# Kernel tuning notes

Measured on AMD Instinct MI355X. Metric: run time of the kernel, lower is better.

The kernel has to match this reference:

```python
import jax, jax.numpy as jnp
import numpy as np

B, N, D, H = 4, 4096, 512, 512
EDGE_P = 0.01  # adjacency density


def _glorot(key, shape):
    fan_in, fan_out = shape
    limit = np.sqrt(6.0 / (fan_in + fan_out)).astype(np.float32)
    return jax.random.uniform(key, shape, jnp.float32, -limit, limit)


def setup_inputs() -> dict:
    key = jax.random.key(0)
    ks = jax.random.split(key, 9)
    batch_graph = jax.random.normal(ks[0], (B, N, D), jnp.float32)
    adj = (jax.random.uniform(ks[1], (B, N, N)) < EDGE_P).astype(jnp.float32)
    adj = jnp.minimum(adj + jnp.eye(N, dtype=jnp.float32)[None], 1.0)  # self loops, 0/1
    return {
        "batch_graph": batch_graph,
        "adj": adj,
        "W1": _glorot(ks[2], (D, H)), "b1": jnp.zeros((H,), jnp.float32),
        "W2": _glorot(ks[3], (H, H)), "b2": jnp.zeros((H,), jnp.float32),
        "W3": _glorot(ks[4], (H, D)), "b3": jnp.zeros((D,), jnp.float32),
    }


def _normalize_adj(adj):
    # Faithful to GCN.normalize_sparse_adj: D^{-1/2} A^T D^{-1/2}
    rowsum = adj.sum(axis=1)                       # [B, N] (sum over dim 1, as in torch)
    d_inv_sqrt = jnp.where(rowsum > 0, jax.lax.rsqrt(jnp.maximum(rowsum, 1e-30)), 0.0)
    # (A @ diag(d))^T @ diag(d)  ->  d_i * A[j,i] * d_j
    return d_inv_sqrt[:, :, None] * jnp.swapaxes(adj, 1, 2) * d_inv_sqrt[:, None, :]


def reference(batch_graph, adj, W1, b1, W2, b2, W3, b3):
    # Block-diagonal big_adj @ big_graph == independent per-batch matmuls;
    # we exploit that instead of materializing the [B*N, B*N] dense matrix.
    a = _normalize_adj(adj)                                   # [B, N, N]
    # GraphConvolution (pygcn-style): out = adj @ (x @ W) + b; dropout = identity (eval)
    h = jax.nn.relu(jnp.einsum('bij,bjd->bid', a, batch_graph @ W1) + b1)
    h = jax.nn.relu(jnp.einsum('bij,bjd->bid', a, h @ W2) + b2)
    out = jnp.einsum('bij,bjd->bid', a, h @ W3) + b3          # [B, N, D]
    return out
```

## Files before the change

kernel.cpp:

```cpp
#include <hip/hip_runtime.h>
#include <stdint.h>

#define CAP 128

typedef __attribute__((ext_vector_type(8))) short bf16x8;
typedef __attribute__((ext_vector_type(4))) float f32x4;

typedef __attribute__((address_space(3))) uint32_t lds_u32;
typedef __attribute__((address_space(1))) const uint32_t glb_u32;

__device__ __forceinline__ unsigned short f2bf(float f) {
  union { float f; uint32_t u; } c; c.f = f;
  return (unsigned short)((c.u + 0x7fffu + ((c.u >> 16) & 1u)) >> 16);
}
__device__ __forceinline__ float bf2f(uint32_t b) {
  union { uint32_t u; float f; } c; c.u = b << 16; return c.f;
}

__global__ __launch_bounds__(256) void k_detect(const uint32_t* __restrict__ a,
                                                int* __restrict__ flag) {
  int i = blockIdx.x * 256 + threadIdx.x;
  bool found = false;
  for (int k = 0; k < 64; k++) {
    uint32_t x = a[(size_t)k * 65536 + i];
    if (x == 0x00003F80u || x == 0x3F803F80u) found = true;
  }
  if (found) flag[0] = 1;
}

__global__ __launch_bounds__(256) void k_build(const void* __restrict__ adjp,
                                               int* __restrict__ cnt,
                                               int* __restrict__ cols,
                                               const int* __restrict__ flag) {
  int gid = blockIdx.x * 256 + threadIdx.x;
  if (flag[0]) {
    const uint4* a = (const uint4*)adjp;
    uint4 v = a[gid];
    int i0 = (gid & 511) * 8;
    int j  = (gid >> 9) & 4095;
    int b  = gid >> 21;
    int base = b << 12;
    uint32_t w[4] = {v.x, v.y, v.z, v.w};
#pragma unroll
    for (int q = 0; q < 4; q++) {
      if (w[q] & 0xffffu) {
        int c = base + i0 + q * 2;
        int p = atomicAdd(&cnt[c], 1);
        if (p < CAP) cols[(size_t)c * CAP + p] = j;
      }
      if (w[q] >> 16) {
        int c = base + i0 + q * 2 + 1;
        int p = atomicAdd(&cnt[c], 1);
        if (p < CAP) cols[(size_t)c * CAP + p] = j;
      }
    }
  } else {
    const float4* a = (const float4*)adjp;
#pragma unroll
    for (int it = 0; it < 2; it++) {
      int v4 = gid + it * 8388608;
      float4 v = a[v4];
      int i0 = (v4 & 1023) * 4;
      int j  = (v4 >> 10) & 4095;
      int b  = v4 >> 22;
      int base = b << 12;
      float e[4] = {v.x, v.y, v.z, v.w};
#pragma unroll
      for (int q = 0; q < 4; q++) {
        if (e[q] != 0.0f) {
          int c = base + i0 + q;
          int p = atomicAdd(&cnt[c], 1);
          if (p < CAP) cols[(size_t)c * CAP + p] = j;
        }
      }
    }
  }
}

__global__ __launch_bounds__(256) void k_dinv(const int* __restrict__ cnt,
                                              float* __restrict__ dinv) {
  int i = blockIdx.x * 256 + threadIdx.x;
  int c = cnt[i];
  dinv[i] = (c > 0) ? 1.0f / sqrtf((float)c) : 0.0f;
}

__global__ __launch_bounds__(256) void k_convx(const void* __restrict__ xp,
                                               ushort* __restrict__ xb,
                                               const int* __restrict__ flag) {
  int gid = blockIdx.x * 256 + threadIdx.x;
  if (flag[0]) {
    const uint4* in = (const uint4*)xp;
    ((uint4*)xb)[gid] = in[gid];
  } else {
    const float4* in = (const float4*)xp;
#pragma unroll
    for (int it = 0; it < 2; it++) {
      int i = gid + it * 1048576;
      float4 v = in[i];
      uint32_t lo = (uint32_t)f2bf(v.x) | ((uint32_t)f2bf(v.y) << 16);
      uint32_t hi = (uint32_t)f2bf(v.z) | ((uint32_t)f2bf(v.w) << 16);
      ((uint2*)xb)[i] = make_uint2(lo, hi);
    }
  }
}

__global__ __launch_bounds__(256) void k_wconv(const void* __restrict__ wp,
                                               ushort* __restrict__ wt,
                                               const int* __restrict__ flag) {
  int o = blockIdx.x * 256 + threadIdx.x;
  int n = o >> 9, k = o & 511;
  if (flag[0]) wt[o] = ((const ushort*)wp)[k * 512 + n];
  else         wt[o] = f2bf(((const float*)wp)[k * 512 + n]);
}

__global__ __launch_bounds__(256) void k_bconv(const void* __restrict__ bp,
                                               float* __restrict__ bf,
                                               const int* __restrict__ flag) {
  int i = blockIdx.x * 256 + threadIdx.x;
  bf[i] = flag[0] ? bf2f(((const ushort*)bp)[i]) : ((const float*)bp)[i];
}

__device__ __forceinline__ void gl_lds16(const ushort* g, ushort* l) {
  __builtin_amdgcn_global_load_lds((glb_u32*)g, (lds_u32*)l, 16, 0, 0);
}

__global__ __launch_bounds__(256) void k_gemm(const ushort* __restrict__ X,
                                              const ushort* __restrict__ WT,
                                              ushort* __restrict__ Z) {
  __shared__ ushort As[128 * 32];
  __shared__ ushort Bs[128 * 32];
  const int K = 512, NO = 512;
  int tid = threadIdx.x;
  int m0 = blockIdx.y * 128, n0 = blockIdx.x * 128;
  int lane = tid & 63;
  int wv = tid >> 6;
  int wm = (wv >> 1) << 6;
  int wn = (wv & 1) << 6;
  int lr = lane & 15;
  int lq = lane >> 4;

  f32x4 zero = {0.f, 0.f, 0.f, 0.f};
  f32x4 acc[4][4];
#pragma unroll
  for (int im = 0; im < 4; im++)
#pragma unroll
    for (int in_ = 0; in_ < 4; in_++) acc[im][in_] = zero;

  const ushort* Xg = X  + (size_t)(m0 + (tid >> 2)) * K + ((tid & 3) << 3);
  const ushort* Wg = WT + (size_t)(n0 + (tid >> 2)) * K + ((tid & 3) << 3);

  for (int kt = 0; kt < K; kt += 32) {
    __syncthreads();
    gl_lds16(Xg + kt,                    &As[tid * 8]);
    gl_lds16(Xg + kt + (size_t)64 * K,   &As[2048 + tid * 8]);
    gl_lds16(Wg + kt,                    &Bs[tid * 8]);
    gl_lds16(Wg + kt + (size_t)64 * K,   &Bs[2048 + tid * 8]);
    __syncthreads();
    bf16x8 af[4], bfr[4];
#pragma unroll
    for (int im = 0; im < 4; im++)
      af[im] = *(const bf16x8*)&As[(wm + im * 16 + lr) * 32 + lq * 8];
#pragma unroll
    for (int in_ = 0; in_ < 4; in_++)
      bfr[in_] = *(const bf16x8*)&Bs[(wn + in_ * 16 + lr) * 32 + lq * 8];
#pragma unroll
    for (int im = 0; im < 4; im++)
#pragma unroll
      for (int in_ = 0; in_ < 4; in_++)
        acc[im][in_] = __builtin_amdgcn_mfma_f32_16x16x32_bf16(
            af[im], bfr[in_], acc[im][in_], 0, 0, 0);
  }

#pragma unroll
  for (int im = 0; im < 4; im++) {
    int row0 = m0 + wm + im * 16 + lq * 4;
#pragma unroll
    for (int in_ = 0; in_ < 4; in_++) {
      int col = n0 + wn + in_ * 16 + lr;
#pragma unroll
      for (int r = 0; r < 4; r++)
        Z[(size_t)(row0 + r) * NO + col] = f2bf(acc[im][in_][r]);
    }
  }
}

__global__ __launch_bounds__(256) void k_spmm(const ushort* __restrict__ Z,
                                              const int* __restrict__ cnt,
                                              const int* __restrict__ cols,
                                              const float* __restrict__ dinv,
                                              const float* __restrict__ bias,
                                              void* __restrict__ outp,
                                              int do_relu, int is_final,
                                              const int* __restrict__ flag) {
  __shared__ int   sj[CAP];
  __shared__ float sv[CAP];
  int r = blockIdx.x;
  int b = r >> 12;
  int t = threadIdx.x;
  int nnz = cnt[r];
  if (nnz > CAP) nnz = CAP;
  if (t < nnz) {
    int j = cols[(size_t)r * CAP + t];
    sj[t] = j;
    sv[t] = dinv[r] * dinv[(b << 12) + j];
  }
  __syncthreads();

  const ushort* Zb = Z + ((size_t)(b << 12)) * 512 + (t << 1);
  float a0 = 0.f, a1 = 0.f;
  int k = 0;
  for (; k + 2 <= nnz; k += 2) {
    int j0 = sj[k], j1 = sj[k + 1];
    float v0 = sv[k], v1 = sv[k + 1];
    uint32_t z0 = *(const uint32_t*)(Zb + (size_t)j0 * 512);
    uint32_t z1 = *(const uint32_t*)(Zb + (size_t)j1 * 512);
    a0 += v0 * bf2f(z0 & 0xffffu);
    a1 += v0 * bf2f(z0 >> 16);
    a0 += v1 * bf2f(z1 & 0xffffu);
    a1 += v1 * bf2f(z1 >> 16);
  }
  if (k < nnz) {
    int j0 = sj[k]; float v0 = sv[k];
    uint32_t z0 = *(const uint32_t*)(Zb + (size_t)j0 * 512);
    a0 += v0 * bf2f(z0 & 0xffffu);
    a1 += v0 * bf2f(z0 >> 16);
  }
  float2 bb = *(const float2*)&bias[t << 1];
  a0 += bb.x; a1 += bb.y;
  if (do_relu) { a0 = fmaxf(a0, 0.f); a1 = fmaxf(a1, 0.f); }

  if (!is_final) {
    *(uint32_t*)((ushort*)outp + (size_t)r * 512 + (t << 1)) =
        (uint32_t)f2bf(a0) | ((uint32_t)f2bf(a1) << 16);
  } else if (flag[0]) {
    *(uint32_t*)((ushort*)outp + (size_t)r * 512 + (t << 1)) =
        (uint32_t)f2bf(a0) | ((uint32_t)f2bf(a1) << 16);
  } else {
    *(float2*)((float*)outp + (size_t)r * 512 + (t << 1)) = make_float2(a0, a1);
  }
}

extern "C" void kernel_launch(void* const* d_in, const int* in_sizes, int n_in,
                              void* d_out, int out_size, void* d_ws, size_t ws_size,
                              hipStream_t stream) {
  const void* X  = d_in[0];
  const void* A  = d_in[1];
  const void* W1 = d_in[2]; const void* b1 = d_in[3];
  const void* W2 = d_in[4]; const void* b2 = d_in[5];
  const void* W3 = d_in[6]; const void* b3 = d_in[7];

  char* ws = (char*)d_ws;
  size_t off = 0;
  auto alloc = [&](size_t bytes) -> void* {
    void* p = ws + off;
    off += (bytes + 255) & ~(size_t)255;
    return p;
  };
  int*    cnt  = (int*)alloc(16384 * 4);
  int*    flag = (int*)alloc(4);
  float*  dinv = (float*)alloc(16384 * 4);
  int*    cols = (int*)alloc((size_t)16384 * CAP * 4);
  ushort* W1T  = (ushort*)alloc(512 * 512 * 2);
  ushort* W2T  = (ushort*)alloc(512 * 512 * 2);
  ushort* W3T  = (ushort*)alloc(512 * 512 * 2);
  float*  b1f  = (float*)alloc(512 * 4);
  float*  b2f  = (float*)alloc(512 * 4);
  float*  b3f  = (float*)alloc(512 * 4);
  ushort* Xb   = (ushort*)alloc((size_t)16384 * 512 * 2);
  ushort* Zb   = (ushort*)alloc((size_t)16384 * 512 * 2);
  ushort* Hb   = (ushort*)alloc((size_t)16384 * 512 * 2);

  hipMemsetAsync(cnt, 0, 65536 + 256, stream);

  k_detect<<<256, 256, 0, stream>>>((const uint32_t*)A, flag);
  k_build<<<32768, 256, 0, stream>>>(A, cnt, cols, flag);
  k_dinv<<<64, 256, 0, stream>>>(cnt, dinv);
  k_convx<<<4096, 256, 0, stream>>>(X, Xb, flag);
  k_wconv<<<1024, 256, 0, stream>>>(W1, W1T, flag);
  k_wconv<<<1024, 256, 0, stream>>>(W2, W2T, flag);
  k_wconv<<<1024, 256, 0, stream>>>(W3, W3T, flag);
  k_bconv<<<2, 256, 0, stream>>>(b1, b1f, flag);
  k_bconv<<<2, 256, 0, stream>>>(b2, b2f, flag);
  k_bconv<<<2, 256, 0, stream>>>(b3, b3f, flag);

  dim3 gg(4, 128);
  k_gemm<<<gg, 256, 0, stream>>>(Xb, W1T, Zb);
  k_spmm<<<16384, 256, 0, stream>>>(Zb, cnt, cols, dinv, b1f, Hb, 1, 0, flag);
  k_gemm<<<gg, 256, 0, stream>>>(Hb, W2T, Zb);
  k_spmm<<<16384, 256, 0, stream>>>(Zb, cnt, cols, dinv, b2f, Xb, 1, 0, flag);
  k_gemm<<<gg, 256, 0, stream>>>(Xb, W3T, Zb);
  k_spmm<<<16384, 256, 0, stream>>>(Zb, cnt, cols, dinv, b3f, d_out, 0, 1, flag);
}
```

Before: 735.8 us.

## Assign one wavefront per SpMM row with 16-byte loads; merge small prep kernels

Restructures the sparse aggregation kernel so each 64-lane wave handles one row with 8 bf16 features per lane via 128-bit loads. Four rows share a block and the block-wide barrier is removed. Small per-weight and per-bias conversion kernels are merged into single launches to cut launch overhead. This relies on intra-wave LDS visibility without an explicit barrier.

Result: faster. 601.1 us (-18.3%).

```diff
diff --git a/kernel.cpp b/kernel.cpp
--- a/kernel.cpp
+++ b/kernel.cpp
@@ -2,6 +2,7 @@
 #include <stdint.h>
 
 #define CAP 128
+#define RPB 4
 
 typedef __attribute__((ext_vector_type(8))) short bf16x8;
 typedef __attribute__((ext_vector_type(4))) float f32x4;
@@ -15,6 +16,9 @@
 }
 __device__ __forceinline__ float bf2f(uint32_t b) {
   union { uint32_t u; float f; } c; c.u = b << 16; return c.f;
+}
+__device__ __forceinline__ float as_f32(uint32_t u) {
+  union { uint32_t u; float f; } c; c.u = u; return c.f;
 }
 
 __global__ __launch_bounds__(256) void k_detect(const uint32_t* __restrict__ a,
@@ -77,11 +81,27 @@
   }
 }
 
-__global__ __launch_bounds__(256) void k_dinv(const int* __restrict__ cnt,
-                                              float* __restrict__ dinv) {
-  int i = blockIdx.x * 256 + threadIdx.x;
-  int c = cnt[i];
-  dinv[i] = (c > 0) ? 1.0f / sqrtf((float)c) : 0.0f;
+__global__ __launch_bounds__(256) void k_prep(const int* __restrict__ cnt,
+                                              float* __restrict__ dinv,
+                                              const void* b1, const void* b2,
+                                              const void* b3,
+                                              float* __restrict__ b1f,
+                                              float* __restrict__ b2f,
+                                              float* __restrict__ b3f,
+                                              const int* __restrict__ flag) {
+  int id = blockIdx.x * 256 + threadIdx.x;
+  if (id < 16384) {
+    int c = cnt[id];
+    dinv[id] = (c > 0) ? 1.0f / sqrtf((float)c) : 0.0f;
+  } else {
+    int o = id - 16384;
+    if (o < 1536) {
+      const void* src = (o < 512) ? b1 : (o < 1024) ? b2 : b3;
+      float* dst = (o < 512) ? b1f : (o < 1024) ? b2f : b3f;
+      int i = o & 511;
+      dst[i] = flag[0] ? bf2f(((const ushort*)src)[i]) : ((const float*)src)[i];
+    }
+  }
 }
 
 __global__ __launch_bounds__(256) void k_convx(const void* __restrict__ xp,
@@ -104,20 +124,20 @@
   }
 }
 
-__global__ __launch_bounds__(256) void k_wconv(const void* __restrict__ wp,
-                                               ushort* __restrict__ wt,
+__global__ __launch_bounds__(256) void k_wconv(const void* w1, const void* w2,
+                                               const void* w3,
+                                               ushort* __restrict__ wt1,
+                                               ushort* __restrict__ wt2,
+                                               ushort* __restrict__ wt3,
                                                const int* __restrict__ flag) {
-  int o = blockIdx.x * 256 + threadIdx.x;
+  int id = blockIdx.x * 256 + threadIdx.x;
+  int w = id >> 18;
+  int o = id & 262143;
+  const void* wp = (w == 0) ? w1 : (w == 1) ? w2 : w3;
+  ushort* wt = (w == 0) ? wt1 : (w == 1) ? wt2 : wt3;
   int n = o >> 9, k = o & 511;
   if (flag[0]) wt[o] = ((const ushort*)wp)[k * 512 + n];
   else         wt[o] = f2bf(((const float*)wp)[k * 512 + n]);
-}
-
-__global__ __launch_bounds__(256) void k_bconv(const void* __restrict__ bp,
-                                               float* __restrict__ bf,
-                                               const int* __restrict__ flag) {
-  int i = blockIdx.x * 256 + threadIdx.x;
-  bf[i] = flag[0] ? bf2f(((const ushort*)bp)[i]) : ((const float*)bp)[i];
 }
 
 __device__ __forceinline__ void gl_lds16(const ushort* g, ushort* l) {
@@ -192,51 +212,75 @@
                                               void* __restrict__ outp,
                                               int do_relu, int is_final,
                                               const int* __restrict__ flag) {
-  __shared__ int   sj[CAP];
-  __shared__ float sv[CAP];
-  int r = blockIdx.x;
-  int b = r >> 12;
-  int t = threadIdx.x;
+  __shared__ int   sj[RPB][CAP];
+  __shared__ float sv[RPB][CAP];
+  int B = blockIdx.x;
+  int wv = threadIdx.x >> 6;
+  int lane = threadIdx.x & 63;
+  int batch = (B & 7) >> 1;
+  int lb = ((B >> 3) << 1) | (B & 1);
+  int r = (batch << 12) + lb * RPB + wv;
+  int base = batch << 12;
+
   int nnz = cnt[r];
   if (nnz > CAP) nnz = CAP;
-  if (t < nnz) {
-    int j = cols[(size_t)r * CAP + t];
-    sj[t] = j;
-    sv[t] = dinv[r] * dinv[(b << 12) + j];
-  }
-  __syncthreads();
-
-  const ushort* Zb = Z + ((size_t)(b << 12)) * 512 + (t << 1);
-  float a0 = 0.f, a1 = 0.f;
+  float dr = dinv[r];
+  for (int k = lane; k < nnz; k += 64) {
+    int j = cols[(size_t)r * CAP + k];
+    sj[wv][k] = j;
+    sv[wv][k] = dr * dinv[base + j];
+  }
+
+  const ushort* Zb = Z + (size_t)base * 512 + lane * 8;
+  const float4* bp = (const float4*)bias + lane * 2;
+  float4 bb0 = bp[0], bb1 = bp[1];
+  float a[8] = {bb0.x, bb0.y, bb0.z, bb0.w, bb1.x, bb1.y, bb1.z, bb1.w};
+
   int k = 0;
   for (; k + 2 <= nnz; k += 2) {
-    int j0 = sj[k], j1 = sj[k + 1];
-    float v0 = sv[k], v1 = sv[k + 1];
-    uint32_t z0 = *(const uint32_t*)(Zb + (size_t)j0 * 512);
-    uint32_t z1 = *(const uint32_t*)(Zb + (size_t)j1 * 512);
-    a0 += v0 * bf2f(z0 & 0xffffu);
-    a1 += v0 * bf2f(z0 >> 16);
-    a0 += v1 * bf2f(z1 & 0xffffu);
-    a1 += v1 * bf2f(z1 >> 16);
+    int j0 = sj[wv][k], j1 = sj[wv][k + 1];
+    float v0 = sv[wv][k], v1 = sv[wv][k + 1];
+    uint4 z0 = *(const uint4*)(Zb + (size_t)j0 * 512);
+    uint4 z1 = *(const uint4*)(Zb + (size_t)j1 * 512);
+    uint32_t w0[4] = {z0.x, z0.y, z0.z, z0.w};
+    uint32_t w1[4] = {z1.x, z1.y, z1.z, z1.w};
+#pragma unroll
+    for (int q = 0; q < 4; q++) {
+      a[q * 2]     += v0 * as_f32(w0[q] << 16);
+      a[q * 2 + 1] += v0 * as_f32(w0[q] & 0xffff0000u);
+      a[q * 2]     += v1 * as_f32(w1[q] << 16);
+      a[q * 2 + 1] += v1 * as_f32(w1[q] & 0xffff0000u);
+    }
   }
   if (k < nnz) {
-    int j0 = sj[k]; float v0 = sv[k];
-    uint32_t z0 = *(const uint32_t*)(Zb + (size_t)j0 * 512);
-    a0 += v0 * bf2f(z0 & 0xffffu);
-    a1 += v0 * bf2f(z0 >> 16);
-  }
-  float2 bb = *(const float2*)&bias[t << 1];
-  a0 += bb.x; a1 += bb.y;
-  if (do_relu) { a0 = fmaxf(a0, 0.f); a1 = fmaxf(a1, 0.f); }
-
-  if (!is_final) {
-    *(uint32_t*)((ushort*)outp + (size_t)r * 512 + (t << 1)) =
-        (uint32_t)f2bf(a0) | ((uint32_t)f2bf(a1) << 16);
-  } else if (flag[0]) {
-    *(uint32_t*)((ushort*)outp + (size_t)r * 512 + (t << 1)) =
-        (uint32_t)f2bf(a0) | ((uint32_t)f2bf(a1) << 16);
+    int j0 = sj[wv][k];
+    float v0 = sv[wv][k];
+    uint4 z0 = *(const uint4*)(Zb + (size_t)j0 * 512);
+    uint32_t w0[4] = {z0.x, z0.y, z0.z, z0.w};
+#pragma unroll
+    for (int q = 0; q < 4; q++) {
+      a[q * 2]     += v0 * as_f32(w0[q] << 16);
+      a[q * 2 + 1] += v0 * as_f32(w0[q] & 0xffff0000u);
+    }
+  }
+
+  if (do_relu) {
+#pragma unroll
+    for (int q = 0; q < 8; q++) a[q] = fmaxf(a[q], 0.f);
+  }
+
+  if (!is_final || flag[0]) {
+    uint4 o;
+    o.x = (uint32_t)f2bf(a[0]) | ((uint32_t)f2bf(a[1]) << 16);
+    o.y = (uint32_t)f2bf(a[2]) | ((uint32_t)f2bf(a[3]) << 16);
+    o.z = (uint32_t)f2bf(a[4]) | ((uint32_t)f2bf(a[5]) << 16);
+    o.w = (uint32_t)f2bf(a[6]) | ((uint32_t)f2bf(a[7]) << 16);
+    *(uint4*)((ushort*)outp + (size_t)r * 512 + lane * 8) = o;
   } else {
-    *(float2*)((float*)outp + (size_t)r * 512 + (t << 1)) = make_float2(a0, a1);
+    float4 o0 = make_float4(a[0], a[1], a[2], a[3]);
+    float4 o1 = make_float4(a[4], a[5], a[6], a[7]);
+    float4* op = (float4*)((float*)outp + (size_t)r * 512 + lane * 8);
+    op[0] = o0; op[1] = o1;
   }
 }
 
@@ -274,20 +318,15 @@
 
   k_detect<<<256, 256, 0, stream>>>((const uint32_t*)A, flag);
   k_build<<<32768, 256, 0, stream>>>(A, cnt, cols, flag);
-  k_dinv<<<64, 256, 0, stream>>>(cnt, dinv);
+  k_prep<<<70, 256, 0, stream>>>(cnt, dinv, b1, b2, b3, b1f, b2f, b3f, flag);
   k_convx<<<4096, 256, 0, stream>>>(X, Xb, flag);
-  k_wconv<<<1024, 256, 0, stream>>>(W1, W1T, flag);
-  k_wconv<<<1024, 256, 0, stream>>>(W2, W2T, flag);
-  k_wconv<<<1024, 256, 0, stream>>>(W3, W3T, flag);
-  k_bconv<<<2, 256, 0, stream>>>(b1, b1f, flag);
-  k_bconv<<<2, 256, 0, stream>>>(b2, b2f, flag);
-  k_bconv<<<2, 256, 0, stream>>>(b3, b3f, flag);
+  k_wconv<<<3072, 256, 0, stream>>>(W1, W2, W3, W1T, W2T, W3T, flag);
 
   dim3 gg(4, 128);
   k_gemm<<<gg, 256, 0, stream>>>(Xb, W1T, Zb);
-  k_spmm<<<16384, 256, 0, stream>>>(Zb, cnt, cols, dinv, b1f, Hb, 1, 0, flag);
+  k_spmm<<<4096, 256, 0, stream>>>(Zb, cnt, cols, dinv, b1f, Hb, 1, 0, flag);
   k_gemm<<<gg, 256, 0, stream>>>(Hb, W2T, Zb);
-  k_spmm<<<16384, 256, 0, stream>>>(Zb, cnt, cols, dinv, b2f, Xb, 1, 0, flag);
+  k_spmm<<<4096, 256, 0, stream>>>(Zb, cnt, cols, dinv, b2f, Xb, 1, 0, flag);
   k_gemm<<<gg, 256, 0, stream>>>(Xb, W3T, Zb);
-  k_spmm<<<16384, 256, 0, stream>>>(Zb, cnt, cols, dinv, b3f, d_out, 0, 1, flag);
-}
+  k_spmm<<<4096, 256, 0, stream>>>(Zb, cnt, cols, dinv, b3f, d_out, 0, 1, flag);
+}
```
